# Kernel tuning notes

Hardware: AMD Instinct MI355X
Metric: run time of the kernel (lower is better)

The kernel has to match this reference:

```python
import jax, jax.numpy as jnp
import numpy as np

B, T, I, H, O = 8192, 128, 28, 200, 10


def setup_inputs() -> dict:
    key = jax.random.key(0)
    ks = jax.random.split(key, 7)
    s_ih = 1.0 / np.sqrt(H)
    return {
        "x": jax.random.normal(ks[0], (B, T, I), dtype=jnp.float32),
        "W_ih": jax.random.uniform(ks[1], (H, I), jnp.float32, -s_ih, s_ih),
        "W_hh": jax.random.uniform(ks[2], (H, H), jnp.float32, -s_ih, s_ih),
        "b_ih": jax.random.uniform(ks[3], (H,), jnp.float32, -s_ih, s_ih),
        "b_hh": jax.random.uniform(ks[4], (H,), jnp.float32, -s_ih, s_ih),
        "W_fc": jax.random.uniform(ks[5], (O, H), jnp.float32, -s_ih, s_ih),
        "b_fc": jax.random.uniform(ks[6], (O,), jnp.float32, -s_ih, s_ih),
    }


def reference(x, W_ih, W_hh, b_ih, b_hh, W_fc, b_fc):
    # Precompute input projections for all timesteps in one GEMM: [B,T,H]
    xp = jnp.einsum("bti,hi->bth", x, W_ih) + b_ih + b_hh
    h0 = jnp.zeros((x.shape[0], W_hh.shape[0]), dtype=x.dtype)

    def step(h, xp_t):
        # h_t = relu(x_t W_ih^T + b_ih + h_{t-1} W_hh^T + b_hh)
        h = jax.nn.relu(xp_t + h @ W_hh.T)
        return h, None

    # scan over time: xp transposed to [T,B,H]
    h_last, _ = jax.lax.scan(step, h0, jnp.swapaxes(xp, 0, 1))
    # out[:, -1, :] then fc1
    return h_last @ W_fc.T + b_fc
```

## Files before the change

kernel.cpp:

```cpp
#include <hip/hip_runtime.h>

typedef float f4v __attribute__((ext_vector_type(4)));
typedef short s8v __attribute__((ext_vector_type(8)));

#define TT 128
#define II 28
#define HH 200
#define BB 16
#define NT 512
#define SH 232
#define XS 40
#define CH 8
#define KX 224
#define NCH (TT / CH)

template <bool B> struct BC { static constexpr bool value = B; };

__device__ __forceinline__ unsigned pk_hu(float a, float b) {
    unsigned ua = __builtin_bit_cast(unsigned, a) + 0x8000u;
    unsigned ub = __builtin_bit_cast(unsigned, b) + 0x8000u;
    return __builtin_amdgcn_perm(ub, ua, 0x07060302);
}
__device__ __forceinline__ short f2bf(float f) {
    return (short)((__builtin_bit_cast(unsigned, f) + 0x8000u) >> 16);
}
__device__ __forceinline__ float bf2f(short s) {
    return __builtin_bit_cast(float, ((unsigned)(unsigned short)s) << 16);
}

#define STEP_BAR() asm volatile("s_waitcnt lgkmcnt(0)\n\ts_barrier" ::: "memory")

__global__ __launch_bounds__(NT, 4)
void rnn_r9(const float* __restrict__ x,
            const float* __restrict__ W_ih,
            const float* __restrict__ W_hh,
            const float* __restrict__ b_ih,
            const float* __restrict__ b_hh,
            const float* __restrict__ W_fc,
            const float* __restrict__ b_fc,
            float* __restrict__ out)
{
    __shared__ __align__(16) short Hs[2][BB][SH];
    __shared__ __align__(16) short Xb[CH][BB][XS];
    __shared__ __align__(16) float Xl[CH * BB * II];

    const int tid  = threadIdx.x;
    const int lane = tid & 63;
    const int q    = lane >> 4;
    const int lr   = lane & 15;
    const int wave = __builtin_amdgcn_readfirstlane(tid >> 6);
    const int b0   = blockIdx.x * BB;

    const bool two = (wave < 5);
    const int jt0  = two ? 2 * wave : 10 + (wave - 5);
    const int jt1  = two ? 2 * wave + 1 : 13;

    const int nIss = (wave < 6) ? 2 : 1;
    const int e0   = (wave < 6) ? 2 * wave : 12 + (wave - 6);
    unsigned xoff[2];
    #pragma unroll
    for (int k = 0; k < 2; ++k) {
        const int e  = e0 + k;
        const int m  = (e << 6) + lane;
        const int tl = m / 112;
        const int rm = m - tl * 112;
        const int r  = rm / 7;
        const int c4 = rm - r * 7;
        xoff[k] = (unsigned)(((((b0 + r) * TT + tl) * II) + c4 * 4) * 4);
    }
    auto issue_dma = [&](int c) {
        #pragma unroll
        for (int k = 0; k < 2; ++k) {
            if (k < nIss) {
                const char* src = (const char*)x + (xoff[k] + (unsigned)c * (CH * II * 4));
                float* dst = &Xl[(e0 + k) * 256];
                __builtin_amdgcn_global_load_lds(
                    (const __attribute__((address_space(1))) void*)src,
                    (__attribute__((address_space(3))) void*)dst, 16, 0, 0);
            }
        }
    };

    issue_dma(0);

    s8v Af[2][8];
    #pragma unroll
    for (int u = 0; u < 2; ++u) {
        const int j = 16 * (u ? jt1 : jt0) + lr;
        #pragma unroll
        for (int kc = 0; kc < 8; ++kc) {
            union { short s[8]; s8v v; } tv;
            #pragma unroll
            for (int i = 0; i < 8; ++i) {
                const int k = 32 * kc + 8 * q + i;
                float w = 0.0f;
                if (j < HH) {
                    if (k < HH)                     w = W_hh[j * HH + k];
                    else if (k >= KX && k < KX+II)  w = W_ih[j * II + (k - KX)];
                    else if (k == KX + II) {
                        w = b_ih[j] + b_hh[j];
                    } else if (k == KX + II + 1) {
                        const float bs = b_ih[j] + b_hh[j];
                        w = bs - bf2f(f2bf(bs));
                    }
                }
                tv.s[i] = f2bf(w);
            }
            Af[u][kc] = tv.v;
        }
    }

    for (int i = tid; i < (2 * BB * SH) / 2; i += NT) ((int*)Hs)[i] = 0;
    for (int i = tid; i < (CH * BB * XS) / 2; i += NT)
        ((int*)Xb)[i] = (i % 20 == 14) ? 0x3f803f80 : 0;

    const f4v Z = {0.f, 0.f, 0.f, 0.f};

    auto steps = [&](auto TWOC) {
        constexpr bool TWO = decltype(TWOC)::value;
        #pragma unroll
        for (int s = 0; s < CH; ++s) {
            const int pb = s & 1;
            const short* hrow = &Hs[pb][lr][8 * q];
            s8v g0 = *(const s8v*)(hrow);
            s8v g1 = *(const s8v*)(hrow + 32);
            s8v g2 = *(const s8v*)(hrow + 64);
            s8v g3 = *(const s8v*)(hrow + 96);
            const s8v xb = *(const s8v*)&Xb[s][lr][8 * q];
            __builtin_amdgcn_s_setprio(1);
            f4v a0 = __builtin_amdgcn_mfma_f32_16x16x32_bf16(Af[0][7], xb, Z, 0, 0, 0);
            f4v a1;
            if constexpr (TWO) a1 = __builtin_amdgcn_mfma_f32_16x16x32_bf16(Af[1][7], xb, Z, 0, 0, 0);
            a0 = __builtin_amdgcn_mfma_f32_16x16x32_bf16(Af[0][0], g0, a0, 0, 0, 0);
            if constexpr (TWO) a1 = __builtin_amdgcn_mfma_f32_16x16x32_bf16(Af[1][0], g0, a1, 0, 0, 0);
            g0 = *(const s8v*)(hrow + 128);
            a0 = __builtin_amdgcn_mfma_f32_16x16x32_bf16(Af[0][1], g1, a0, 0, 0, 0);
            if constexpr (TWO) a1 = __builtin_amdgcn_mfma_f32_16x16x32_bf16(Af[1][1], g1, a1, 0, 0, 0);
            g1 = *(const s8v*)(hrow + 160);
            a0 = __builtin_amdgcn_mfma_f32_16x16x32_bf16(Af[0][2], g2, a0, 0, 0, 0);
            if constexpr (TWO) a1 = __builtin_amdgcn_mfma_f32_16x16x32_bf16(Af[1][2], g2, a1, 0, 0, 0);
            g2 = *(const s8v*)(hrow + 192);
            a0 = __builtin_amdgcn_mfma_f32_16x16x32_bf16(Af[0][3], g3, a0, 0, 0, 0);
            if constexpr (TWO) a1 = __builtin_amdgcn_mfma_f32_16x16x32_bf16(Af[1][3], g3, a1, 0, 0, 0);
            a0 = __builtin_amdgcn_mfma_f32_16x16x32_bf16(Af[0][4], g0, a0, 0, 0, 0);
            if constexpr (TWO) a1 = __builtin_amdgcn_mfma_f32_16x16x32_bf16(Af[1][4], g0, a1, 0, 0, 0);
            a0 = __builtin_amdgcn_mfma_f32_16x16x32_bf16(Af[0][5], g1, a0, 0, 0, 0);
            if constexpr (TWO) a1 = __builtin_amdgcn_mfma_f32_16x16x32_bf16(Af[1][5], g1, a1, 0, 0, 0);
            a0 = __builtin_amdgcn_mfma_f32_16x16x32_bf16(Af[0][6], g2, a0, 0, 0, 0);
            if constexpr (TWO) a1 = __builtin_amdgcn_mfma_f32_16x16x32_bf16(Af[1][6], g2, a1, 0, 0, 0);
            __builtin_amdgcn_s_setprio(0);
            {
                const int wb = pb ^ 1;
                int2 hv;
                hv.x = (int)pk_hu(fmaxf(a0.x, 0.f), fmaxf(a0.y, 0.f));
                hv.y = (int)pk_hu(fmaxf(a0.z, 0.f), fmaxf(a0.w, 0.f));
                *(int2*)&Hs[wb][lr][16 * jt0 + 4 * q] = hv;
                if constexpr (TWO) {
                    hv.x = (int)pk_hu(fmaxf(a1.x, 0.f), fmaxf(a1.y, 0.f));
                    hv.y = (int)pk_hu(fmaxf(a1.z, 0.f), fmaxf(a1.w, 0.f));
                    *(int2*)&Hs[wb][lr][16 * jt1 + 4 * q] = hv;
                }
            }
            if (s < CH - 1) STEP_BAR();
        }
    };

    #pragma unroll 1
    for (int c = 0; c < NCH; ++c) {
        __syncthreads();
        if (tid < 448) {
            const f4v v0 = *(const f4v*)&Xl[tid * 8];
            const f4v v1 = *(const f4v*)&Xl[tid * 8 + 4];
            const unsigned d[4] = { pk_hu(v0.x, v0.y), pk_hu(v0.z, v0.w),
                                    pk_hu(v1.x, v1.y), pk_hu(v1.z, v1.w) };
            #pragma unroll
            for (int dk = 0; dk < 4; ++dk) {
                const int kk = tid * 4 + dk;
                const int t  = kk / 224;
                const int k2 = kk - t * 224;
                const int r  = k2 / 14;
                const int cp = k2 - r * 14;
                ((int*)Xb)[t * 320 + r * 20 + cp] = (int)d[dk];
            }
        }
        STEP_BAR();
        if (c + 1 < NCH) issue_dma(c + 1);
        if (two) steps(BC<true>{});
        else     steps(BC<false>{});
    }

    __syncthreads();
    if (tid < BB * 10) {
        const int o = tid >> 4, r = tid & 15;
        const float* wrow = W_fc + o * HH;
        float acc = b_fc[o];
        #pragma unroll 1
        for (int kb = 0; kb < 25; ++kb) {
            const s8v hv = *(const s8v*)&Hs[0][r][kb * 8];
            const f4v w0 = *(const f4v*)(wrow + kb * 8);
            const f4v w1 = *(const f4v*)(wrow + kb * 8 + 4);
            acc = fmaf(bf2f(hv[0]), w0.x, acc);
            acc = fmaf(bf2f(hv[1]), w0.y, acc);
            acc = fmaf(bf2f(hv[2]), w0.z, acc);
            acc = fmaf(bf2f(hv[3]), w0.w, acc);
            acc = fmaf(bf2f(hv[4]), w1.x, acc);
            acc = fmaf(bf2f(hv[5]), w1.y, acc);
            acc = fmaf(bf2f(hv[6]), w1.z, acc);
            acc = fmaf(bf2f(hv[7]), w1.w, acc);
        }
        __builtin_nontemporal_store(acc, &out[(long)(b0 + r) * 10 + o]);
    }
}

extern "C" void kernel_launch(void* const* d_in, const int* in_sizes, int n_in,
                              void* d_out, int out_size, void* d_ws, size_t ws_size,
                              hipStream_t stream) {
    const float* x    = (const float*)d_in[0];
    const float* W_ih = (const float*)d_in[1];
    const float* W_hh = (const float*)d_in[2];
    const float* b_ih = (const float*)d_in[3];
    const float* b_hh = (const float*)d_in[4];
    const float* W_fc = (const float*)d_in[5];
    const float* b_fc = (const float*)d_in[6];
    float* out = (float*)d_out;

    rnn_r9<<<dim3(8192 / BB), dim3(NT), 0, stream>>>(
        x, W_ih, W_hh, b_ih, b_hh, W_fc, b_fc, out);
}
```

Before: 289.3 us.

## Double-buffer bf16 input chunks and overlap conversion/DMA with recurrence steps

Double-buffers the bf16 packed input tile so that converting the next chunk and issuing its DMA happen inside the current chunk's timestep loop. This removes the per-chunk __syncthreads and serialized conversion phase. Single-tile waves now split their K reduction into two independent MFMA chains, which shortens the dependency chain. The s_setprio hints are dropped. The DMA is now two chunks ahead, and a vmcnt wait at step 3 guards the reuse of Xl. This ordering is subtle and could race if the wait placement is wrong.

```diff
diff --git a/kernel.cpp b/kernel.cpp
--- a/kernel.cpp
+++ b/kernel.cpp
@@ -29,19 +29,20 @@
 }
 
 #define STEP_BAR() asm volatile("s_waitcnt lgkmcnt(0)\n\ts_barrier" ::: "memory")
+#define VSTEP_BAR() asm volatile("s_waitcnt vmcnt(0) lgkmcnt(0)\n\ts_barrier" ::: "memory")
 
 __global__ __launch_bounds__(NT, 4)
-void rnn_r9(const float* __restrict__ x,
-            const float* __restrict__ W_ih,
-            const float* __restrict__ W_hh,
-            const float* __restrict__ b_ih,
-            const float* __restrict__ b_hh,
-            const float* __restrict__ W_fc,
-            const float* __restrict__ b_fc,
-            float* __restrict__ out)
+void rnn_r10(const float* __restrict__ x,
+             const float* __restrict__ W_ih,
+             const float* __restrict__ W_hh,
+             const float* __restrict__ b_ih,
+             const float* __restrict__ b_hh,
+             const float* __restrict__ W_fc,
+             const float* __restrict__ b_fc,
+             float* __restrict__ out)
 {
     __shared__ __align__(16) short Hs[2][BB][SH];
-    __shared__ __align__(16) short Xb[CH][BB][XS];
+    __shared__ __align__(16) short Xb[2][CH][BB][XS];
     __shared__ __align__(16) float Xl[CH * BB * II];
 
     const int tid  = threadIdx.x;
@@ -77,6 +78,25 @@
                 __builtin_amdgcn_global_load_lds(
                     (const __attribute__((address_space(1))) void*)src,
                     (__attribute__((address_space(3))) void*)dst, 16, 0, 0);
+            }
+        }
+    };
+
+    auto prepass = [&](int tc) {
+        if (tid < 448) {
+            const f4v v0 = *(const f4v*)&Xl[tid * 8];
+            const f4v v1 = *(const f4v*)&Xl[tid * 8 + 4];
+            const unsigned d[4] = { pk_hu(v0.x, v0.y), pk_hu(v0.z, v0.w),
+                                    pk_hu(v1.x, v1.y), pk_hu(v1.z, v1.w) };
+            int* dstb = ((int*)Xb) + (tc & 1) * 2560;
+            #pragma unroll
+            for (int dk = 0; dk < 4; ++dk) {
+                const int kk = tid * 4 + dk;
+                const int t  = kk / 224;
+                const int k2 = kk - t * 224;
+                const int r  = k2 / 14;
+                const int cp = k2 - r * 14;
+                dstb[t * 320 + r * 20 + cp] = (int)d[dk];
             }
         }
     };
@@ -111,44 +131,67 @@
     }
 
     for (int i = tid; i < (2 * BB * SH) / 2; i += NT) ((int*)Hs)[i] = 0;
-    for (int i = tid; i < (CH * BB * XS) / 2; i += NT)
+    for (int i = tid; i < (2 * CH * BB * XS) / 2; i += NT)
         ((int*)Xb)[i] = (i % 20 == 14) ? 0x3f803f80 : 0;
 
+    __syncthreads();
+    prepass(0);
+    STEP_BAR();
+    issue_dma(1);
+
     const f4v Z = {0.f, 0.f, 0.f, 0.f};
 
-    auto steps = [&](auto TWOC) {
+    auto chunk = [&](int c, auto TWOC) {
         constexpr bool TWO = decltype(TWOC)::value;
+        const short* xbase = &Xb[c & 1][0][0][0];
         #pragma unroll
         for (int s = 0; s < CH; ++s) {
             const int pb = s & 1;
             const short* hrow = &Hs[pb][lr][8 * q];
-            s8v g0 = *(const s8v*)(hrow);
-            s8v g1 = *(const s8v*)(hrow + 32);
-            s8v g2 = *(const s8v*)(hrow + 64);
-            s8v g3 = *(const s8v*)(hrow + 96);
-            const s8v xb = *(const s8v*)&Xb[s][lr][8 * q];
-            __builtin_amdgcn_s_setprio(1);
-            f4v a0 = __builtin_amdgcn_mfma_f32_16x16x32_bf16(Af[0][7], xb, Z, 0, 0, 0);
-            f4v a1;
-            if constexpr (TWO) a1 = __builtin_amdgcn_mfma_f32_16x16x32_bf16(Af[1][7], xb, Z, 0, 0, 0);
-            a0 = __builtin_amdgcn_mfma_f32_16x16x32_bf16(Af[0][0], g0, a0, 0, 0, 0);
-            if constexpr (TWO) a1 = __builtin_amdgcn_mfma_f32_16x16x32_bf16(Af[1][0], g0, a1, 0, 0, 0);
-            g0 = *(const s8v*)(hrow + 128);
-            a0 = __builtin_amdgcn_mfma_f32_16x16x32_bf16(Af[0][1], g1, a0, 0, 0, 0);
-            if constexpr (TWO) a1 = __builtin_amdgcn_mfma_f32_16x16x32_bf16(Af[1][1], g1, a1, 0, 0, 0);
-            g1 = *(const s8v*)(hrow + 160);
-            a0 = __builtin_amdgcn_mfma_f32_16x16x32_bf16(Af[0][2], g2, a0, 0, 0, 0);
-            if constexpr (TWO) a1 = __builtin_amdgcn_mfma_f32_16x16x32_bf16(Af[1][2], g2, a1, 0, 0, 0);
-            g2 = *(const s8v*)(hrow + 192);
-            a0 = __builtin_amdgcn_mfma_f32_16x16x32_bf16(Af[0][3], g3, a0, 0, 0, 0);
-            if constexpr (TWO) a1 = __builtin_amdgcn_mfma_f32_16x16x32_bf16(Af[1][3], g3, a1, 0, 0, 0);
-            a0 = __builtin_amdgcn_mfma_f32_16x16x32_bf16(Af[0][4], g0, a0, 0, 0, 0);
-            if constexpr (TWO) a1 = __builtin_amdgcn_mfma_f32_16x16x32_bf16(Af[1][4], g0, a1, 0, 0, 0);
-            a0 = __builtin_amdgcn_mfma_f32_16x16x32_bf16(Af[0][5], g1, a0, 0, 0, 0);
-            if constexpr (TWO) a1 = __builtin_amdgcn_mfma_f32_16x16x32_bf16(Af[1][5], g1, a1, 0, 0, 0);
-            a0 = __builtin_amdgcn_mfma_f32_16x16x32_bf16(Af[0][6], g2, a0, 0, 0, 0);
-            if constexpr (TWO) a1 = __builtin_amdgcn_mfma_f32_16x16x32_bf16(Af[1][6], g2, a1, 0, 0, 0);
-            __builtin_amdgcn_s_setprio(0);
+            const s8v xb = *(const s8v*)&xbase[s * (BB * XS) + lr * XS + 8 * q];
+            f4v a0, a1;
+            if constexpr (TWO) {
+                s8v g0 = *(const s8v*)(hrow);
+                s8v g1 = *(const s8v*)(hrow + 32);
+                s8v g2 = *(const s8v*)(hrow + 64);
+                s8v g3 = *(const s8v*)(hrow + 96);
+                a0 = __builtin_amdgcn_mfma_f32_16x16x32_bf16(Af[0][7], xb, Z, 0, 0, 0);
+                a1 = __builtin_amdgcn_mfma_f32_16x16x32_bf16(Af[1][7], xb, Z, 0, 0, 0);
+                a0 = __builtin_amdgcn_mfma_f32_16x16x32_bf16(Af[0][0], g0, a0, 0, 0, 0);
+                a1 = __builtin_amdgcn_mfma_f32_16x16x32_bf16(Af[1][0], g0, a1, 0, 0, 0);
+                g0 = *(const s8v*)(hrow + 128);
+                a0 = __builtin_amdgcn_mfma_f32_16x16x32_bf16(Af[0][1], g1, a0, 0, 0, 0);
+                a1 = __builtin_amdgcn_mfma_f32_16x16x32_bf16(Af[1][1], g1, a1, 0, 0, 0);
+                g1 = *(const s8v*)(hrow + 160);
+                a0 = __builtin_amdgcn_mfma_f32_16x16x32_bf16(Af[0][2], g2, a0, 0, 0, 0);
+                a1 = __builtin_amdgcn_mfma_f32_16x16x32_bf16(Af[1][2], g2, a1, 0, 0, 0);
+                g2 = *(const s8v*)(hrow + 192);
+                a0 = __builtin_amdgcn_mfma_f32_16x16x32_bf16(Af[0][3], g3, a0, 0, 0, 0);
+                a1 = __builtin_amdgcn_mfma_f32_16x16x32_bf16(Af[1][3], g3, a1, 0, 0, 0);
+                a0 = __builtin_amdgcn_mfma_f32_16x16x32_bf16(Af[0][4], g0, a0, 0, 0, 0);
+                a1 = __builtin_amdgcn_mfma_f32_16x16x32_bf16(Af[1][4], g0, a1, 0, 0, 0);
+                a0 = __builtin_amdgcn_mfma_f32_16x16x32_bf16(Af[0][5], g1, a0, 0, 0, 0);
+                a1 = __builtin_amdgcn_mfma_f32_16x16x32_bf16(Af[1][5], g1, a1, 0, 0, 0);
+                a0 = __builtin_amdgcn_mfma_f32_16x16x32_bf16(Af[0][6], g2, a0, 0, 0, 0);
+                a1 = __builtin_amdgcn_mfma_f32_16x16x32_bf16(Af[1][6], g2, a1, 0, 0, 0);
+            } else {
+                s8v g0 = *(const s8v*)(hrow);
+                s8v g1 = *(const s8v*)(hrow + 96);
+                s8v g2 = *(const s8v*)(hrow + 128);
+                s8v g3 = *(const s8v*)(hrow + 160);
+                a0 = __builtin_amdgcn_mfma_f32_16x16x32_bf16(Af[0][7], xb, Z, 0, 0, 0);
+                a1 = __builtin_amdgcn_mfma_f32_16x16x32_bf16(Af[0][3], g1, Z, 0, 0, 0);
+                g1 = *(const s8v*)(hrow + 32);
+                a0 = __builtin_amdgcn_mfma_f32_16x16x32_bf16(Af[0][0], g0, a0, 0, 0, 0);
+                g0 = *(const s8v*)(hrow + 64);
+                a1 = __builtin_amdgcn_mfma_f32_16x16x32_bf16(Af[0][4], g2, a1, 0, 0, 0);
+                g2 = *(const s8v*)(hrow + 192);
+                a0 = __builtin_amdgcn_mfma_f32_16x16x32_bf16(Af[0][1], g1, a0, 0, 0, 0);
+                a1 = __builtin_amdgcn_mfma_f32_16x16x32_bf16(Af[0][5], g3, a1, 0, 0, 0);
+                a0 = __builtin_amdgcn_mfma_f32_16x16x32_bf16(Af[0][2], g0, a0, 0, 0, 0);
+                a1 = __builtin_amdgcn_mfma_f32_16x16x32_bf16(Af[0][6], g2, a1, 0, 0, 0);
+                a0 += a1;
+            }
             {
                 const int wb = pb ^ 1;
                 int2 hv;
@@ -161,32 +204,17 @@
                     *(int2*)&Hs[wb][lr][16 * jt1 + 4 * q] = hv;
                 }
             }
-            if (s < CH - 1) STEP_BAR();
+            if (s == 4 && c + 1 < NCH) prepass(c + 1);
+            if (s == 5 && c + 2 < NCH) issue_dma(c + 2);
+            if (s == 3) VSTEP_BAR();
+            else        STEP_BAR();
         }
     };
 
     #pragma unroll 1
     for (int c = 0; c < NCH; ++c) {
-        __syncthreads();
-        if (tid < 448) {
-            const f4v v0 = *(const f4v*)&Xl[tid * 8];
-            const f4v v1 = *(const f4v*)&Xl[tid * 8 + 4];
-            const unsigned d[4] = { pk_hu(v0.x, v0.y), pk_hu(v0.z, v0.w),
-                                    pk_hu(v1.x, v1.y), pk_hu(v1.z, v1.w) };
-            #pragma unroll
-            for (int dk = 0; dk < 4; ++dk) {
-                const int kk = tid * 4 + dk;
-                const int t  = kk / 224;
-                const int k2 = kk - t * 224;
-                const int r  = k2 / 14;
-                const int cp = k2 - r * 14;
-                ((int*)Xb)[t * 320 + r * 20 + cp] = (int)d[dk];
-            }
-        }
-        STEP_BAR();
-        if (c + 1 < NCH) issue_dma(c + 1);
-        if (two) steps(BC<true>{});
-        else     steps(BC<false>{});
+        if (two) chunk(c, BC<true>{});
+        else     chunk(c, BC<false>{});
     }
 
     __syncthreads();
@@ -224,6 +252,6 @@
     const float* b_fc = (const float*)d_in[6];
     float* out = (float*)d_out;
 
-    rnn_r9<<<dim3(8192 / BB), dim3(NT), 0, stream>>>(
+    rnn_r10<<<dim3(8192 / BB), dim3(NT), 0, stream>>>(
         x, W_ih, W_hh, b_ih, b_hh, W_fc, b_fc, out);
 }
```

New measurement: 286.6 us. Within noise of the previous version (-0.9%).
